# Optimization experiments

Measured on AMD Instinct MI355X. Metric: run time of the kernel, lower is better.

Reference implementation:

```python
import jax, jax.numpy as jnp
import numpy as np

N_NODES = 100000
N_EDGES = 1600000
IN_CH, HID_CH, OUT_CH = 128, 64, 32


def setup_inputs() -> dict:
    key = jax.random.key(0)
    k1, k2, k3, k4 = jax.random.split(key, 4)
    x = jax.random.normal(k1, (N_NODES, IN_CH), dtype=jnp.float32)
    edge_index = jax.random.randint(k2, (2, N_EDGES), 0, N_NODES, dtype=jnp.int32)
    # Glorot-ish scaling like PyG's GCNConv init
    W1 = jax.random.normal(k3, (IN_CH, HID_CH), dtype=jnp.float32) / np.sqrt(IN_CH)
    b1 = jnp.zeros((HID_CH,), dtype=jnp.float32)
    W2 = jax.random.normal(k4, (HID_CH, OUT_CH), dtype=jnp.float32) / np.sqrt(HID_CH)
    b2 = jnp.zeros((OUT_CH,), dtype=jnp.float32)
    return {"x": x, "edge_index": edge_index, "W1": W1, "b1": b1, "W2": W2, "b2": b2}


def reference(x, edge_index, W1, b1, W2, b2):
    # PyG GCNConv semantics: add self-loops, symmetric deg^{-1/2} normalization,
    # linear transform, scatter-add aggregation to destination nodes, add bias.
    N = x.shape[0]
    loops = jnp.arange(N, dtype=edge_index.dtype)
    src = jnp.concatenate([edge_index[0], loops])  # [E+N]
    dst = jnp.concatenate([edge_index[1], loops])  # [E+N]

    deg = jax.ops.segment_sum(jnp.ones_like(src, dtype=x.dtype), dst, num_segments=N)
    dis = jnp.where(deg > 0, jax.lax.rsqrt(jnp.maximum(deg, 1.0)), 0.0)  # deg^{-1/2}
    norm = (dis[src] * dis[dst])[:, None]  # [E+N, 1]

    def gcn_conv(h, W, b):
        h = h @ W                                   # [N, C_out]
        msgs = h[src] * norm                        # gather + scale, [E+N, C_out]
        return jax.ops.segment_sum(msgs, dst, num_segments=N) + b

    h = jax.nn.relu(gcn_conv(x, W1, b1))
    # dropout is identity in eval mode (training=False)
    return gcn_conv(h, W2, b2)
```

## Files before the change

kernel.cpp:

```cpp
#include <hip/hip_runtime.h>
#include <hip/hip_bf16.h>

#define IN_CH 128
#define HID_CH 64
#define OUT_CH 32
#define EPB 2048
#define MAXB 512

typedef unsigned short ushort_t;
typedef __attribute__((ext_vector_type(8))) short short8;
typedef __attribute__((ext_vector_type(4))) float float4v;

static __device__ __forceinline__ ushort_t f2bf(float f) {
    unsigned u = __float_as_uint(f);
    unsigned r = (u + 0x7fff + ((u >> 16) & 1)) >> 16;
    return (ushort_t)r;
}
static __device__ __forceinline__ float bf_lo(unsigned u) { return __uint_as_float(u << 16); }
static __device__ __forceinline__ float bf_hi(unsigned u) { return __uint_as_float(u & 0xffff0000u); }


__global__ __launch_bounds__(256) void k_partition(const int* __restrict__ src,
                                                   const int* __restrict__ dst,
                                                   int* __restrict__ gcursor,
                                                   unsigned* __restrict__ pairs,
                                                   int E, int nbk, int cap) {
    __shared__ int lhist[MAXB];
    __shared__ int lbase[MAXB];
    __shared__ int lcur[MAXB];
    const int tid = threadIdx.x;
    for (int b = tid; b < nbk; b += 256) { lhist[b] = 0; lcur[b] = 0; }
    __syncthreads();
    int s[8], d[8];
    const int e0 = blockIdx.x * EPB;
#pragma unroll
    for (int j = 0; j < 8; ++j) {
        int e = e0 + j * 256 + tid;
        if (e < E) {
            s[j] = src[e];
            d[j] = dst[e];
            atomicAdd(&lhist[d[j] >> 8], 1);
        } else {
            d[j] = -1;
        }
    }
    __syncthreads();
    for (int b = tid; b < nbk; b += 256)
        lbase[b] = lhist[b] ? atomicAdd(&gcursor[b], lhist[b]) : 0;
    __syncthreads();
#pragma unroll
    for (int j = 0; j < 8; ++j) {
        if (d[j] >= 0) {
            int b = d[j] >> 8;
            int loc = atomicAdd(&lcur[b], 1);
            int idx = lbase[b] + loc;
            if (idx < cap)
                pairs[(long long)b * cap + idx] = ((unsigned)s[j] << 8) | (unsigned)(d[j] & 255);
        }
    }
}

__global__ __launch_bounds__(512) void k_bscan(const int* __restrict__ gcursor,
                                               int* __restrict__ bbase,
                                               int* __restrict__ rowptr,
                                               int nbk, int cap, int N) {
    __shared__ int s[512];
    const int tid = threadIdx.x;
    int v = (tid < nbk) ? min(gcursor[tid], cap) : 0;
    s[tid] = v;
    __syncthreads();
    for (int off = 1; off < 512; off <<= 1) {
        int val = (tid >= off) ? s[tid - off] : 0;
        __syncthreads();
        s[tid] += val;
        __syncthreads();
    }
    if (tid < nbk) bbase[tid] = s[tid] - v;
    if (tid == nbk - 1) rowptr[N] = s[tid];
}

__global__ __launch_bounds__(256) void k_bucket_build(const unsigned* __restrict__ pairs,
                                                      const int* __restrict__ gcursor,
                                                      const int* __restrict__ bbase,
                                                      int* __restrict__ rowptr,
                                                      int* __restrict__ col,
                                                      float* __restrict__ dis,
                                                      int cap, int N) {
    __shared__ int lc[256];
    __shared__ int ls[256];
    __shared__ int lcur[256];
    const int b = blockIdx.x, tid = threadIdx.x;
    lc[tid] = 0;
    __syncthreads();
    const int cnt = min(gcursor[b], cap);
    const int base = bbase[b];
    const unsigned* p = pairs + (long long)b * cap;
    for (int i = tid; i < cnt; i += 256) atomicAdd(&lc[p[i] & 255], 1);
    __syncthreads();
    const int v = lc[tid];
    ls[tid] = v;
    __syncthreads();
    for (int off = 1; off < 256; off <<= 1) {
        int val = (tid >= off) ? ls[tid - off] : 0;
        __syncthreads();
        ls[tid] += val;
        __syncthreads();
    }
    const int excl = ls[tid] - v;
    const int row = b * 256 + tid;
    if (row < N) {
        rowptr[row] = base + excl;
        dis[row] = rsqrtf((float)(v + 1));
    }
    lcur[tid] = base + excl;
    __syncthreads();
    for (int i = tid; i < cnt; i += 256) {
        unsigned pk = p[i];
        int pos = atomicAdd(&lcur[pk & 255], 1);
        col[pos] = (int)(pk >> 8);
    }
}


__global__ __launch_bounds__(256) void k_prepW(const float* __restrict__ W,
                                               unsigned* __restrict__ wsW,
                                               int* __restrict__ gcursor) {
    int s = blockIdx.x * 256 + threadIdx.x;
    if (s < MAXB) gcursor[s] = 0;
    if (s >= 1024) return;
    int lane = s & 63;
    int nt = (s >> 6) & 3;
    int kc = s >> 8;
    int c = nt * 16 + (lane & 15);
    int k0 = kc * 32 + (lane >> 4) * 8;
    unsigned o[4];
#pragma unroll
    for (int d = 0; d < 4; ++d) {
        unsigned lo = f2bf(W[(k0 + 2 * d) * 64 + c]);
        unsigned hi = f2bf(W[(k0 + 2 * d + 1) * 64 + c]);
        o[d] = lo | (hi << 16);
    }
    ((uint4*)wsW)[s] = make_uint4(o[0], o[1], o[2], o[3]);
}


__global__ __launch_bounds__(256) void k_mm1(const float* __restrict__ X,
                                             const unsigned* __restrict__ wsW,
                                             ushort_t* __restrict__ H, int N) {
    const int tid = threadIdx.x;
    const int wv = tid >> 6, lane = tid & 63;
    const int quad = lane >> 4, n16 = lane & 15;
    const int rowbase = blockIdx.x * 64 + wv * 16;
    const int myrow = rowbase + n16;
    const bool rok = (myrow < N);

    float4v acc0 = {}, acc1 = {}, acc2 = {}, acc3 = {};

#pragma unroll
    for (int kc = 0; kc < 4; ++kc) {
        float4 xa = make_float4(0.f, 0.f, 0.f, 0.f), xb = xa;
        if (rok) {
            const float4* p = (const float4*)(X + (long long)myrow * 128 + kc * 32 + quad * 8);
            xa = p[0];
            xb = p[1];
        }
        unsigned pk[4];
        pk[0] = (unsigned)f2bf(xa.x) | ((unsigned)f2bf(xa.y) << 16);
        pk[1] = (unsigned)f2bf(xa.z) | ((unsigned)f2bf(xa.w) << 16);
        pk[2] = (unsigned)f2bf(xb.x) | ((unsigned)f2bf(xb.y) << 16);
        pk[3] = (unsigned)f2bf(xb.z) | ((unsigned)f2bf(xb.w) << 16);
        short8 a;
        a[0] = (short)(pk[0] & 0xffff); a[1] = (short)(pk[0] >> 16);
        a[2] = (short)(pk[1] & 0xffff); a[3] = (short)(pk[1] >> 16);
        a[4] = (short)(pk[2] & 0xffff); a[5] = (short)(pk[2] >> 16);
        a[6] = (short)(pk[3] & 0xffff); a[7] = (short)(pk[3] >> 16);

        const short8* wb = (const short8*)wsW;
        short8 b0 = wb[(kc * 4 + 0) * 64 + lane];
        short8 b1 = wb[(kc * 4 + 1) * 64 + lane];
        short8 b2 = wb[(kc * 4 + 2) * 64 + lane];
        short8 b3 = wb[(kc * 4 + 3) * 64 + lane];

        acc0 = __builtin_amdgcn_mfma_f32_16x16x32_bf16(a, b0, acc0, 0, 0, 0);
        acc1 = __builtin_amdgcn_mfma_f32_16x16x32_bf16(a, b1, acc1, 0, 0, 0);
        acc2 = __builtin_amdgcn_mfma_f32_16x16x32_bf16(a, b2, acc2, 0, 0, 0);
        acc3 = __builtin_amdgcn_mfma_f32_16x16x32_bf16(a, b3, acc3, 0, 0, 0);
    }

#pragma unroll
    for (int i = 0; i < 4; ++i) {
        int row = rowbase + quad * 4 + i;
        if (row < N) {
            long long o = (long long)row * 64 + n16;
            H[o]      = f2bf(acc0[i]);
            H[o + 16] = f2bf(acc1[i]);
            H[o + 32] = f2bf(acc2[i]);
            H[o + 48] = f2bf(acc3[i]);
        }
    }
}


__global__ __launch_bounds__(256) void k_agg64_mm2(const unsigned* __restrict__ h,
                                                   const int* __restrict__ rowptr,
                                                   const int* __restrict__ col,
                                                   const float* __restrict__ dis,
                                                   const float* __restrict__ b1,
                                                   const float* __restrict__ W2,
                                                   unsigned* __restrict__ h2, int N) {
    __shared__ float zbuf[4][64];
    const int wv = threadIdx.x >> 6, lane = threadIdx.x & 63;
    const int t = lane & 31, g = lane >> 5;

    float w[32];
#pragma unroll
    for (int k = 0; k < 32; ++k) w[k] = W2[(g * 32 + k) * 32 + t];
    const float2 bv = ((const float2*)b1)[t];

    const int wave0 = blockIdx.x * 4 + wv;
    const int nwaves = gridDim.x * 4;

    for (int row = wave0; row < N; row += nwaves) {
        const int start = rowptr[row];
        const int deg = rowptr[row + 1] - start;
        const float dr = dis[row];

        int myCol = row;
        float myDis = 0.f;
        if (lane < deg) {
            myCol = col[start + lane];
            myDis = dis[myCol];
        }

        unsigned us = h[row * 32 + t];
        float w0s = g ? 0.f : dr;
        float ax = w0s * bf_lo(us), ay = w0s * bf_hi(us);

        const int cnt = min(deg, 64);
        for (int k0 = 0; k0 < cnt; k0 += 16) {
#pragma unroll
            for (int u = 0; u < 8; ++u) {
                int slot = k0 + 2 * u + g;
                int s = __shfl(myCol, slot);
                float ww = __shfl(myDis, slot);
                unsigned uu = h[s * 32 + t];
                ax += ww * bf_lo(uu);
                ay += ww * bf_hi(uu);
            }
        }
        for (int j = start + 64 + g; j < start + deg; j += 2) {
            int s = col[j];
            float ww = dis[s];
            unsigned uu = h[s * 32 + t];
            ax += ww * bf_lo(uu);
            ay += ww * bf_hi(uu);
        }
        ax += __shfl_down(ax, 32);
        ay += __shfl_down(ay, 32);

        if (!g) {
            float2 zv;
            zv.x = bv.x + dr * ax;
            zv.y = bv.y + dr * ay;
            *(float2*)&zbuf[wv][2 * t] = zv;
        }
        __builtin_amdgcn_wave_barrier();

        float acc = 0.f;
        const float* zp = &zbuf[wv][g * 32];
#pragma unroll
        for (int k = 0; k < 32; k += 4) {
            float4 zv = *(const float4*)(zp + k);
            acc += fmaxf(zv.x, 0.f) * w[k] + fmaxf(zv.y, 0.f) * w[k + 1] +
                   fmaxf(zv.z, 0.f) * w[k + 2] + fmaxf(zv.w, 0.f) * w[k + 3];
        }
        __builtin_amdgcn_wave_barrier();
        acc += __shfl_down(acc, 32);

        float o0 = __shfl(acc, 2 * t);
        float o1 = __shfl(acc, 2 * t + 1);
        if (lane < 16)
            h2[row * 16 + lane] = (unsigned)f2bf(o0) | ((unsigned)f2bf(o1) << 16);
    }
}


__global__ __launch_bounds__(256) void k_agg32(const unsigned* __restrict__ h,
                                               const int* __restrict__ rowptr,
                                               const int* __restrict__ col,
                                               const float* __restrict__ dis,
                                               const float* __restrict__ b,
                                               float* __restrict__ out, int N) {
    const int wave = (blockIdx.x * 256 + threadIdx.x) >> 6;
    const int lane = threadIdx.x & 63;
    if (wave >= N) return;
    const int row = wave;
    const int t = lane & 15, g = lane >> 4;
    const int start = rowptr[row];
    const int deg = rowptr[row + 1] - start;
    const float dr = dis[row];

    int myCol = row;
    float myDis = 0.f;
    if (lane < deg) {
        myCol = col[start + lane];
        myDis = dis[myCol];
    }

    unsigned us = h[row * 16 + t];
    float w0s = (g == 0) ? dr : 0.f;
    float ax = w0s * bf_lo(us), ay = w0s * bf_hi(us);

    const int cnt = min(deg, 64);
    for (int k0 = 0; k0 < cnt; k0 += 32) {
#pragma unroll
        for (int u = 0; u < 8; ++u) {
            int slot = k0 + 4 * u + g;
            int s = __shfl(myCol, slot);
            float w = __shfl(myDis, slot);
            unsigned uu = h[s * 16 + t];
            ax += w * bf_lo(uu);
            ay += w * bf_hi(uu);
        }
    }
    for (int j = start + 64 + g; j < start + deg; j += 4) {
        int s = col[j];
        float w = dis[s];
        unsigned uu = h[s * 16 + t];
        ax += w * bf_lo(uu);
        ay += w * bf_hi(uu);
    }
    ax += __shfl_down(ax, 32);
    ay += __shfl_down(ay, 32);
    ax += __shfl_down(ax, 16);
    ay += __shfl_down(ay, 16);
    if (!g) {
        float2 bv = ((const float2*)b)[t];
        float2 o;
        o.x = bv.x + dr * ax;
        o.y = bv.y + dr * ay;
        ((float2*)out)[row * 16 + t] = o;
    }
}

extern "C" void kernel_launch(void* const* d_in, const int* in_sizes, int n_in,
                              void* d_out, int out_size, void* d_ws, size_t ws_size,
                              hipStream_t stream) {
    const float* x  = (const float*)d_in[0];
    const int*   ei = (const int*)d_in[1];
    const float* W1 = (const float*)d_in[2];
    const float* b1 = (const float*)d_in[3];
    const float* W2 = (const float*)d_in[4];
    const float* b2 = (const float*)d_in[5];
    float* out = (float*)d_out;

    const int N = in_sizes[0] / IN_CH;
    const int E = in_sizes[1] / 2;
    const int* esrc = ei;
    const int* edst = ei + E;

    int nbk = (N + 255) >> 8;
    if (nbk > MAXB) nbk = MAXB;
    const int per_b = (E + nbk - 1) / nbk;
    const int cap = per_b + per_b / 4 + 256;

    int* rowptr   = (int*)d_ws;
    int* gcursor  = rowptr + (((N + 1) + 15) & ~15);
    int* bbase    = gcursor + MAXB;
    unsigned* wsW = (unsigned*)(bbase + MAXB);
    int* col      = (int*)(wsW + 4096);
    float* dis    = (float*)(col + ((E + 15) & ~15));
    ushort_t* h1  = (ushort_t*)(dis + ((N + 15) & ~15));
    unsigned* scratch = (unsigned*)(h1 + (((long long)N * 64 + 31) & ~31LL));
    unsigned* pairs = scratch;
    unsigned* h2    = scratch;

    const int B = 256;

    k_prepW<<<4, B, 0, stream>>>(W1, wsW, gcursor);
    k_partition<<<(E + EPB - 1) / EPB, B, 0, stream>>>(esrc, edst, gcursor, pairs, E, nbk, cap);
    k_bscan<<<1, 512, 0, stream>>>(gcursor, bbase, rowptr, nbk, cap, N);
    k_bucket_build<<<nbk, B, 0, stream>>>(pairs, gcursor, bbase, rowptr, col, dis, cap, N);

    k_mm1<<<(N + 63) / 64, B, 0, stream>>>(x, wsW, h1, N);

    const int fblocks = (N + 31) / 32;
    k_agg64_mm2<<<fblocks, B, 0, stream>>>((const unsigned*)h1, rowptr, col, dis, b1, W2, h2, N);

    k_agg32<<<((long long)N * 64 + B - 1) / B, B, 0, stream>>>((const unsigned*)h2, rowptr, col, dis, b2, out, N);
}
```

Before: 251.8 us.

## Process two rows per wave in aggregation kernels and fold small setup kernels

Both aggregation kernels now have each wavefront handle two destination rows at once. The two rows' gathers are interleaved to expose more independent memory loads per wave, and the second layer uses half the waves. The separate bucket-scan kernel is removed: every bucket-build block recomputes the global bucket prefix sum itself. W1 preparation is folded into extra blocks of the partition kernel, and the cursor reset becomes a memset. This cuts launches and raises memory-level parallelism, at the cost of more registers, redundant scans, and imbalance when paired rows differ in degree.

```diff
diff --git a/kernel.cpp b/kernel.cpp
--- a/kernel.cpp
+++ b/kernel.cpp
@@ -24,11 +24,32 @@
                                                    const int* __restrict__ dst,
                                                    int* __restrict__ gcursor,
                                                    unsigned* __restrict__ pairs,
-                                                   int E, int nbk, int cap) {
+                                                   int E, int nbk, int cap, int PB,
+                                                   const float* __restrict__ W1,
+                                                   unsigned* __restrict__ wsW) {
     __shared__ int lhist[MAXB];
     __shared__ int lbase[MAXB];
     __shared__ int lcur[MAXB];
     const int tid = threadIdx.x;
+
+    if (blockIdx.x >= PB) {
+        int s = (blockIdx.x - PB) * 256 + tid;
+        int lane = s & 63;
+        int nt = (s >> 6) & 3;
+        int kc = s >> 8;
+        int c = nt * 16 + (lane & 15);
+        int k0 = kc * 32 + (lane >> 4) * 8;
+        unsigned o[4];
+#pragma unroll
+        for (int d = 0; d < 4; ++d) {
+            unsigned lo = f2bf(W1[(k0 + 2 * d) * 64 + c]);
+            unsigned hi = f2bf(W1[(k0 + 2 * d + 1) * 64 + c]);
+            o[d] = lo | (hi << 16);
+        }
+        ((uint4*)wsW)[s] = make_uint4(o[0], o[1], o[2], o[3]);
+        return;
+    }
+
     for (int b = tid; b < nbk; b += 256) { lhist[b] = 0; lcur[b] = 0; }
     __syncthreads();
     int s[8], d[8];
@@ -60,28 +81,9 @@
     }
 }
 
-__global__ __launch_bounds__(512) void k_bscan(const int* __restrict__ gcursor,
-                                               int* __restrict__ bbase,
-                                               int* __restrict__ rowptr,
-                                               int nbk, int cap, int N) {
-    __shared__ int s[512];
-    const int tid = threadIdx.x;
-    int v = (tid < nbk) ? min(gcursor[tid], cap) : 0;
-    s[tid] = v;
-    __syncthreads();
-    for (int off = 1; off < 512; off <<= 1) {
-        int val = (tid >= off) ? s[tid - off] : 0;
-        __syncthreads();
-        s[tid] += val;
-        __syncthreads();
-    }
-    if (tid < nbk) bbase[tid] = s[tid] - v;
-    if (tid == nbk - 1) rowptr[N] = s[tid];
-}
 
 __global__ __launch_bounds__(256) void k_bucket_build(const unsigned* __restrict__ pairs,
                                                       const int* __restrict__ gcursor,
-                                                      const int* __restrict__ bbase,
                                                       int* __restrict__ rowptr,
                                                       int* __restrict__ col,
                                                       float* __restrict__ dis,
@@ -90,15 +92,10 @@
     __shared__ int ls[256];
     __shared__ int lcur[256];
     const int b = blockIdx.x, tid = threadIdx.x;
-    lc[tid] = 0;
-    __syncthreads();
-    const int cnt = min(gcursor[b], cap);
-    const int base = bbase[b];
-    const unsigned* p = pairs + (long long)b * cap;
-    for (int i = tid; i < cnt; i += 256) atomicAdd(&lc[p[i] & 255], 1);
-    __syncthreads();
-    const int v = lc[tid];
-    ls[tid] = v;
+
+    int ga = min(gcursor[2 * tid], cap);
+    int gb = min(gcursor[2 * tid + 1], cap);
+    ls[tid] = ga + gb;
     __syncthreads();
     for (int off = 1; off < 256; off <<= 1) {
         int val = (tid >= off) ? ls[tid - off] : 0;
@@ -106,6 +103,27 @@
         ls[tid] += val;
         __syncthreads();
     }
+    const int p = b >> 1;
+    const int base = (p ? ls[p - 1] : 0) + ((b & 1) ? min(gcursor[b - 1], cap) : 0);
+    const int total = ls[255];
+    __syncthreads();
+    if (b == 0 && tid == 0) rowptr[N] = total;
+
+    lc[tid] = 0;
+    __syncthreads();
+    const int cnt = min(gcursor[b], cap);
+    const unsigned* pp = pairs + (long long)b * cap;
+    for (int i = tid; i < cnt; i += 256) atomicAdd(&lc[pp[i] & 255], 1);
+    __syncthreads();
+    const int v = lc[tid];
+    ls[tid] = v;
+    __syncthreads();
+    for (int off = 1; off < 256; off <<= 1) {
+        int val = (tid >= off) ? ls[tid - off] : 0;
+        __syncthreads();
+        ls[tid] += val;
+        __syncthreads();
+    }
     const int excl = ls[tid] - v;
     const int row = b * 256 + tid;
     if (row < N) {
@@ -115,32 +133,10 @@
     lcur[tid] = base + excl;
     __syncthreads();
     for (int i = tid; i < cnt; i += 256) {
-        unsigned pk = p[i];
+        unsigned pk = pp[i];
         int pos = atomicAdd(&lcur[pk & 255], 1);
         col[pos] = (int)(pk >> 8);
     }
-}
-
-
-__global__ __launch_bounds__(256) void k_prepW(const float* __restrict__ W,
-                                               unsigned* __restrict__ wsW,
-                                               int* __restrict__ gcursor) {
-    int s = blockIdx.x * 256 + threadIdx.x;
-    if (s < MAXB) gcursor[s] = 0;
-    if (s >= 1024) return;
-    int lane = s & 63;
-    int nt = (s >> 6) & 3;
-    int kc = s >> 8;
-    int c = nt * 16 + (lane & 15);
-    int k0 = kc * 32 + (lane >> 4) * 8;
-    unsigned o[4];
-#pragma unroll
-    for (int d = 0; d < 4; ++d) {
-        unsigned lo = f2bf(W[(k0 + 2 * d) * 64 + c]);
-        unsigned hi = f2bf(W[(k0 + 2 * d + 1) * 64 + c]);
-        o[d] = lo | (hi << 16);
-    }
-    ((uint4*)wsW)[s] = make_uint4(o[0], o[1], o[2], o[3]);
 }
 
 
@@ -208,7 +204,7 @@
                                                    const float* __restrict__ b1,
                                                    const float* __restrict__ W2,
                                                    unsigned* __restrict__ h2, int N) {
-    __shared__ float zbuf[4][64];
+    __shared__ float zbuf[4][2][64];
     const int wv = threadIdx.x >> 6, lane = threadIdx.x & 63;
     const int t = lane & 31, g = lane >> 5;
 
@@ -220,67 +216,89 @@
     const int wave0 = blockIdx.x * 4 + wv;
     const int nwaves = gridDim.x * 4;
 
-    for (int row = wave0; row < N; row += nwaves) {
-        const int start = rowptr[row];
-        const int deg = rowptr[row + 1] - start;
-        const float dr = dis[row];
-
-        int myCol = row;
-        float myDis = 0.f;
-        if (lane < deg) {
-            myCol = col[start + lane];
-            myDis = dis[myCol];
-        }
-
-        unsigned us = h[row * 32 + t];
-        float w0s = g ? 0.f : dr;
-        float ax = w0s * bf_lo(us), ay = w0s * bf_hi(us);
-
-        const int cnt = min(deg, 64);
-        for (int k0 = 0; k0 < cnt; k0 += 16) {
+    for (int r0 = wave0 * 2; r0 < N; r0 += nwaves * 2) {
+        const int r1 = r0, r2 = r0 + 1;
+        const bool has2 = (r2 < N);
+        const int start1 = rowptr[r1];
+        const int deg1 = rowptr[r1 + 1] - start1;
+        int start2 = start1, deg2 = 0;
+        if (has2) { start2 = rowptr[r2]; deg2 = rowptr[r2 + 1] - start2; }
+        const float dr1 = dis[r1];
+        const float dr2 = has2 ? dis[r2] : 0.f;
+
+        int c1 = r1, c2 = r1;
+        float e1 = 0.f, e2 = 0.f;
+        if (lane < deg1) { c1 = col[start1 + lane]; e1 = dis[c1]; }
+        if (lane < deg2) { c2 = col[start2 + lane]; e2 = dis[c2]; }
+
+        unsigned us1 = h[r1 * 32 + t];
+        unsigned us2 = h[(has2 ? r2 : r1) * 32 + t];
+        float w01 = g ? 0.f : dr1, w02 = g ? 0.f : dr2;
+        float ax1 = w01 * bf_lo(us1), ay1 = w01 * bf_hi(us1);
+        float ax2 = w02 * bf_lo(us2), ay2 = w02 * bf_hi(us2);
+
+        const int cntm = min(max(deg1, deg2), 64);
+        for (int k0 = 0; k0 < cntm; k0 += 16) {
 #pragma unroll
             for (int u = 0; u < 8; ++u) {
                 int slot = k0 + 2 * u + g;
-                int s = __shfl(myCol, slot);
-                float ww = __shfl(myDis, slot);
-                unsigned uu = h[s * 32 + t];
-                ax += ww * bf_lo(uu);
-                ay += ww * bf_hi(uu);
+                int s1 = __shfl(c1, slot);
+                float f1 = __shfl(e1, slot);
+                int s2 = __shfl(c2, slot);
+                float f2 = __shfl(e2, slot);
+                unsigned u1 = h[s1 * 32 + t];
+                unsigned u2 = h[s2 * 32 + t];
+                ax1 += f1 * bf_lo(u1); ay1 += f1 * bf_hi(u1);
+                ax2 += f2 * bf_lo(u2); ay2 += f2 * bf_hi(u2);
             }
         }
-        for (int j = start + 64 + g; j < start + deg; j += 2) {
+        for (int j = start1 + 64 + g; j < start1 + deg1; j += 2) {
             int s = col[j];
-            float ww = dis[s];
+            float f = dis[s];
             unsigned uu = h[s * 32 + t];
-            ax += ww * bf_lo(uu);
-            ay += ww * bf_hi(uu);
-        }
-        ax += __shfl_down(ax, 32);
-        ay += __shfl_down(ay, 32);
+            ax1 += f * bf_lo(uu); ay1 += f * bf_hi(uu);
+        }
+        for (int j = start2 + 64 + g; j < start2 + deg2; j += 2) {
+            int s = col[j];
+            float f = dis[s];
+            unsigned uu = h[s * 32 + t];
+            ax2 += f * bf_lo(uu); ay2 += f * bf_hi(uu);
+        }
+        ax1 += __shfl_down(ax1, 32); ay1 += __shfl_down(ay1, 32);
+        ax2 += __shfl_down(ax2, 32); ay2 += __shfl_down(ay2, 32);
 
         if (!g) {
-            float2 zv;
-            zv.x = bv.x + dr * ax;
-            zv.y = bv.y + dr * ay;
-            *(float2*)&zbuf[wv][2 * t] = zv;
+            float2 z1v, z2v;
+            z1v.x = bv.x + dr1 * ax1; z1v.y = bv.y + dr1 * ay1;
+            z2v.x = bv.x + dr2 * ax2; z2v.y = bv.y + dr2 * ay2;
+            *(float2*)&zbuf[wv][0][2 * t] = z1v;
+            *(float2*)&zbuf[wv][1][2 * t] = z2v;
         }
         __builtin_amdgcn_wave_barrier();
 
-        float acc = 0.f;
-        const float* zp = &zbuf[wv][g * 32];
+        float a1 = 0.f, a2 = 0.f;
+        const float* zp1 = &zbuf[wv][0][g * 32];
+        const float* zp2 = &zbuf[wv][1][g * 32];
 #pragma unroll
         for (int k = 0; k < 32; k += 4) {
-            float4 zv = *(const float4*)(zp + k);
-            acc += fmaxf(zv.x, 0.f) * w[k] + fmaxf(zv.y, 0.f) * w[k + 1] +
-                   fmaxf(zv.z, 0.f) * w[k + 2] + fmaxf(zv.w, 0.f) * w[k + 3];
+            float4 zv = *(const float4*)(zp1 + k);
+            a1 += fmaxf(zv.x, 0.f) * w[k] + fmaxf(zv.y, 0.f) * w[k + 1] +
+                  fmaxf(zv.z, 0.f) * w[k + 2] + fmaxf(zv.w, 0.f) * w[k + 3];
+            float4 zw = *(const float4*)(zp2 + k);
+            a2 += fmaxf(zw.x, 0.f) * w[k] + fmaxf(zw.y, 0.f) * w[k + 1] +
+                  fmaxf(zw.z, 0.f) * w[k + 2] + fmaxf(zw.w, 0.f) * w[k + 3];
         }
         __builtin_amdgcn_wave_barrier();
-        acc += __shfl_down(acc, 32);
-
-        float o0 = __shfl(acc, 2 * t);
-        float o1 = __shfl(acc, 2 * t + 1);
+        a1 += __shfl_down(a1, 32);
+        a2 += __shfl_down(a2, 32);
+
+        const int tt = lane & 15;
+        float o0 = __shfl(a1, 2 * tt), o1 = __shfl(a1, 2 * tt + 1);
+        float p0 = __shfl(a2, 2 * tt), p1 = __shfl(a2, 2 * tt + 1);
         if (lane < 16)
-            h2[row * 16 + lane] = (unsigned)f2bf(o0) | ((unsigned)f2bf(o1) << 16);
+            h2[r1 * 16 + lane] = (unsigned)f2bf(o0) | ((unsigned)f2bf(o1) << 16);
+        else if (lane < 32 && has2)
+            h2[r2 * 16 + tt] = (unsigned)f2bf(p0) | ((unsigned)f2bf(p1) << 16);
     }
 }
 
@@ -293,53 +311,73 @@
                                                float* __restrict__ out, int N) {
     const int wave = (blockIdx.x * 256 + threadIdx.x) >> 6;
     const int lane = threadIdx.x & 63;
-    if (wave >= N) return;
-    const int row = wave;
+    const int r1 = 2 * wave, r2 = r1 + 1;
+    if (r1 >= N) return;
+    const bool has2 = (r2 < N);
     const int t = lane & 15, g = lane >> 4;
-    const int start = rowptr[row];
-    const int deg = rowptr[row + 1] - start;
-    const float dr = dis[row];
-
-    int myCol = row;
-    float myDis = 0.f;
-    if (lane < deg) {
-        myCol = col[start + lane];
-        myDis = dis[myCol];
-    }
-
-    unsigned us = h[row * 16 + t];
-    float w0s = (g == 0) ? dr : 0.f;
-    float ax = w0s * bf_lo(us), ay = w0s * bf_hi(us);
-
-    const int cnt = min(deg, 64);
-    for (int k0 = 0; k0 < cnt; k0 += 32) {
+
+    const int start1 = rowptr[r1];
+    const int deg1 = rowptr[r1 + 1] - start1;
+    int start2 = start1, deg2 = 0;
+    if (has2) { start2 = rowptr[r2]; deg2 = rowptr[r2 + 1] - start2; }
+    const float dr1 = dis[r1];
+    const float dr2 = has2 ? dis[r2] : 0.f;
+
+    int c1 = r1, c2 = r1;
+    float e1 = 0.f, e2 = 0.f;
+    if (lane < deg1) { c1 = col[start1 + lane]; e1 = dis[c1]; }
+    if (lane < deg2) { c2 = col[start2 + lane]; e2 = dis[c2]; }
+
+    unsigned us1 = h[r1 * 16 + t];
+    unsigned us2 = h[(has2 ? r2 : r1) * 16 + t];
+    float w01 = (g == 0) ? dr1 : 0.f, w02 = (g == 0) ? dr2 : 0.f;
+    float ax1 = w01 * bf_lo(us1), ay1 = w01 * bf_hi(us1);
+    float ax2 = w02 * bf_lo(us2), ay2 = w02 * bf_hi(us2);
+
+    const int cntm = min(max(deg1, deg2), 64);
+    for (int k0 = 0; k0 < cntm; k0 += 32) {
 #pragma unroll
         for (int u = 0; u < 8; ++u) {
             int slot = k0 + 4 * u + g;
-            int s = __shfl(myCol, slot);
-            float w = __shfl(myDis, slot);
-            unsigned uu = h[s * 16 + t];
-            ax += w * bf_lo(uu);
-            ay += w * bf_hi(uu);
-        }
-    }
-    for (int j = start + 64 + g; j < start + deg; j += 4) {
+            int s1 = __shfl(c1, slot);
+            float f1 = __shfl(e1, slot);
+            int s2 = __shfl(c2, slot);
+            float f2 = __shfl(e2, slot);
+            unsigned u1 = h[s1 * 16 + t];
+            unsigned u2 = h[s2 * 16 + t];
+            ax1 += f1 * bf_lo(u1); ay1 += f1 * bf_hi(u1);
+            ax2 += f2 * bf_lo(u2); ay2 += f2 * bf_hi(u2);
+        }
+    }
+    for (int j = start1 + 64 + g; j < start1 + deg1; j += 4) {
         int s = col[j];
-        float w = dis[s];
+        float f = dis[s];
         unsigned uu = h[s * 16 + t];
-        ax += w * bf_lo(uu);
-        ay += w * bf_hi(uu);
-    }
-    ax += __shfl_down(ax, 32);
-    ay += __shfl_down(ay, 32);
-    ax += __shfl_down(ax, 16);
-    ay += __shfl_down(ay, 16);
-    if (!g) {
-        float2 bv = ((const float2*)b)[t];
+        ax1 += f * bf_lo(uu); ay1 += f * bf_hi(uu);
+    }
+    for (int j = start2 + 64 + g; j < start2 + deg2; j += 4) {
+        int s = col[j];
+        float f = dis[s];
+        unsigned uu = h[s * 16 + t];
+        ax2 += f * bf_lo(uu); ay2 += f * bf_hi(uu);
+    }
+    ax1 += __shfl_down(ax1, 32); ay1 += __shfl_down(ay1, 32);
+    ax1 += __shfl_down(ax1, 16); ay1 += __shfl_down(ay1, 16);
+    ax2 += __shfl_down(ax2, 32); ay2 += __shfl_down(ay2, 32);
+    ax2 += __shfl_down(ax2, 16); ay2 += __shfl_down(ay2, 16);
+
+    float bx2 = __shfl(ax2, t), by2 = __shfl(ay2, t);
+    const float2 bv = ((const float2*)b)[t];
+    if (g == 0) {
         float2 o;
-        o.x = bv.x + dr * ax;
-        o.y = bv.y + dr * ay;
-        ((float2*)out)[row * 16 + t] = o;
+        o.x = bv.x + dr1 * ax1;
+        o.y = bv.y + dr1 * ay1;
+        ((float2*)out)[(long long)r1 * 16 + t] = o;
+    } else if (g == 1 && has2) {
+        float2 o;
+        o.x = bv.x + dr2 * bx2;
+        o.y = bv.y + dr2 * by2;
+        ((float2*)out)[(long long)r2 * 16 + t] = o;
     }
 }
 
@@ -366,8 +404,7 @@
 
     int* rowptr   = (int*)d_ws;
     int* gcursor  = rowptr + (((N + 1) + 15) & ~15);
-    int* bbase    = gcursor + MAXB;
-    unsigned* wsW = (unsigned*)(bbase + MAXB);
+    unsigned* wsW = (unsigned*)(gcursor + MAXB);
     int* col      = (int*)(wsW + 4096);
     float* dis    = (float*)(col + ((E + 15) & ~15));
     ushort_t* h1  = (ushort_t*)(dis + ((N + 15) & ~15));
@@ -376,16 +413,17 @@
     unsigned* h2    = scratch;
 
     const int B = 256;
-
-    k_prepW<<<4, B, 0, stream>>>(W1, wsW, gcursor);
-    k_partition<<<(E + EPB - 1) / EPB, B, 0, stream>>>(esrc, edst, gcursor, pairs, E, nbk, cap);
-    k_bscan<<<1, 512, 0, stream>>>(gcursor, bbase, rowptr, nbk, cap, N);
-    k_bucket_build<<<nbk, B, 0, stream>>>(pairs, gcursor, bbase, rowptr, col, dis, cap, N);
+    const int PB = (E + EPB - 1) / EPB;
+
+    hipMemsetAsync(gcursor, 0, MAXB * sizeof(int), stream);
+    k_partition<<<PB + 4, B, 0, stream>>>(esrc, edst, gcursor, pairs, E, nbk, cap, PB, W1, wsW);
+    k_bucket_build<<<nbk, B, 0, stream>>>(pairs, gcursor, rowptr, col, dis, cap, N);
 
     k_mm1<<<(N + 63) / 64, B, 0, stream>>>(x, wsW, h1, N);
 
     const int fblocks = (N + 31) / 32;
     k_agg64_mm2<<<fblocks, B, 0, stream>>>((const unsigned*)h1, rowptr, col, dis, b1, W2, h2, N);
 
-    k_agg32<<<((long long)N * 64 + B - 1) / B, B, 0, stream>>>((const unsigned*)h2, rowptr, col, dis, b2, out, N);
-}
+    const long long waves32 = (N + 1) / 2;
+    k_agg32<<<(int)((waves32 * 64 + B - 1) / B), B, 0, stream>>>((const unsigned*)h2, rowptr, col, dis, b2, out, N);
+}
```

New measurement: 256.0 us. Within noise of the previous version (+1.7%).
